# Performance work log

Hardware: AMD Instinct MI355X
Metric: run time of the kernel (lower is better)

Reference implementation:

```python
import jax, jax.numpy as jnp
import numpy as np

NUM_GROUPS = 32
EPS = 1e-5  # torch GroupNorm default


def group_norm(x, gamma, beta):
    # x: [B, C, T, H, W]; normalize each (b, t) frame per channel-group (CausalNormalize)
    B, C, T, H, W = x.shape
    xg = x.reshape(B, NUM_GROUPS, C // NUM_GROUPS, T, H, W)
    mu = xg.mean(axis=(2, 4, 5), keepdims=True)
    var = xg.var(axis=(2, 4, 5), keepdims=True)
    xn = ((xg - mu) * jax.lax.rsqrt(var + EPS)).reshape(B, C, T, H, W)
    return xn * gamma[None, :, None, None, None] + beta[None, :, None, None, None]


def setup_inputs() -> dict:
    key = jax.random.key(0)
    ks = jax.random.split(key, 8)
    B, C, T, H, W = 2, 512, 16, 32, 32
    S, D = 64, 1024  # context_T = 4 * T, context_dim
    wscale = 0.02
    return {
        "x": jax.random.normal(ks[0], (B, C, T, H, W), jnp.float32),
        "context": jax.random.normal(ks[1], (B, S, D), jnp.float32),
        "gamma": jnp.ones((C,), jnp.float32),
        "beta": jnp.zeros((C,), jnp.float32),
        "wq": jax.random.normal(ks[2], (C, C), jnp.float32) * wscale,
        "bq": jnp.zeros((C,), jnp.float32),
        "wkv": jax.random.normal(ks[3], (2 * C, D), jnp.float32) * wscale,
        "bkv": jnp.zeros((2 * C,), jnp.float32),
        "wo": jax.random.normal(ks[4], (C, C), jnp.float32) * wscale,
        "bo": jnp.zeros((C,), jnp.float32),
    }


def reference(x, context, gamma, beta, wq, bq, wkv, bkv, wo, bo):
    B, C, T, H, W = x.shape
    S = context.shape[1]
    n = S // T  # context frames per x frame (assert S % T == 0 in original)

    h = group_norm(x, gamma, beta)
    # q_proj: CausalConv3d with kernel 1, padding 0 == pointwise channel linear
    q = jnp.einsum('bcthw,oc->bothw', h, wq) + bq[None, :, None, None, None]

    kv = jnp.einsum('bsd,od->bso', context, wkv) + bkv  # [B, S, 2C]
    k, v = jnp.split(kv, 2, axis=-1)                    # each [B, S, C]

    # space2batch: [B,C,T,H,W] -> [B, H*W, T, C] (batch-major, queries per spatial pos)
    qb = q.transpose(0, 3, 4, 2, 1).reshape(B, H * W, T, C)

    # attention; kv broadcast over H*W done implicitly via einsum
    scores = jnp.einsum('bptc,bsc->bpts', qb, k) * (C ** -0.5)
    # block-causal mask: row i attends to context positions < (i+1)*n
    mask = jnp.arange(S)[None, :] < jnp.minimum((jnp.arange(T) + 1) * n, S)[:, None]
    scores = jnp.where(mask[None, None], scores, -jnp.inf)
    w = jax.nn.softmax(scores, axis=-1)
    o = jnp.einsum('bpts,bsc->bptc', w, v)              # [B, HW, T, C]

    # batch2space: back to [B, C, T, H, W]
    o = o.reshape(B, H, W, T, C).transpose(0, 4, 3, 1, 2)
    o = jnp.einsum('bcthw,oc->bothw', o, wo) + bo[None, :, None, None, None]
    return x + o
```

## Files before the change

### kernel.cpp

```cpp
#include <hip/hip_runtime.h>


typedef float    f32x4 __attribute__((ext_vector_type(4)));
typedef _Float16 half8 __attribute__((ext_vector_type(8)));
typedef _Float16 half4 __attribute__((ext_vector_type(4)));

#define GLB_AS __attribute__((address_space(1)))
#define LDS_AS __attribute__((address_space(3)))

__device__ __forceinline__ void gload_lds16(const void* g, void* l) {
  __builtin_amdgcn_global_load_lds((const GLB_AS void*)g, (LDS_AS void*)l, 16, 0, 0);
}

__global__ __launch_bounds__(256) void gn_stats(const float* __restrict__ x,
                                                float* __restrict__ muA,
                                                float* __restrict__ rsA)
{
  const int t = blockIdx.x, g = blockIdx.y, b = blockIdx.z;
  const int tid = threadIdx.x;
  float s1 = 0.f, s2 = 0.f;
#pragma unroll
  for (int c = 0; c < 16; ++c) {
    const long base = (((long)(b * 512 + g * 16 + c) * 16 + t) << 10) + tid * 4;
    const f32x4 v = *(const f32x4*)&x[base];
    s1 += v[0] + v[1] + v[2] + v[3];
    s2 += v[0] * v[0] + v[1] * v[1] + v[2] * v[2] + v[3] * v[3];
  }
  for (int o = 32; o; o >>= 1) { s1 += __shfl_down(s1, o); s2 += __shfl_down(s2, o); }
  __shared__ float r1[4], r2[4];
  const int w = tid >> 6;
  if ((tid & 63) == 0) { r1[w] = s1; r2[w] = s2; }
  __syncthreads();
  if (tid == 0) {
    const float a = r1[0] + r1[1] + r1[2] + r1[3];
    const float q = r2[0] + r2[1] + r2[2] + r2[3];
    const float mu = a * (1.f / 16384.f);
    const float var = q * (1.f / 16384.f) - mu * mu;
    const int idx = (b * 32 + g) * 16 + t;
    muA[idx] = mu;
    rsA[idx] = 1.f / sqrtf(var + 1e-5f);
  }
}

__global__ __launch_bounds__(256) void gn_apply(const float* __restrict__ x,
                                                const float* __restrict__ muA,
                                                const float* __restrict__ rsA,
                                                const float* __restrict__ gamma,
                                                const float* __restrict__ beta,
                                                _Float16* __restrict__ h)
{
  const int b = blockIdx.z;
  const int c0 = blockIdx.y * 64;
  const int p0 = blockIdx.x * 64;
  const int t = p0 >> 10;
  __shared__ float tile[64 * 65];
  const int tid = threadIdx.x;
  const int rr = tid >> 4;
  const int col4 = (tid & 15) * 4;
#pragma unroll
  for (int i = 0; i < 4; ++i) {
    const int r = i * 16 + rr;
    const int c = c0 + r;
    const int gi = (b * 32 + (c >> 4)) * 16 + t;
    const float s = rsA[gi] * gamma[c];
    const float o = beta[c] - muA[gi] * s;
    const f32x4 v = *(const f32x4*)&x[(((long)b * 512 + c) << 14) + p0 + col4];
    tile[r * 65 + col4 + 0] = v[0] * s + o;
    tile[r * 65 + col4 + 1] = v[1] * s + o;
    tile[r * 65 + col4 + 2] = v[2] * s + o;
    tile[r * 65 + col4 + 3] = v[3] * s + o;
  }
  __syncthreads();
  const int pr = tid >> 2;
  const int cs = (tid & 3) * 16;
  const long obase = (((long)b * 16384 + p0 + pr) << 9) + c0 + cs;
  half8 h0, h1;
#pragma unroll
  for (int j = 0; j < 16; ++j) {
    const _Float16 hi = (_Float16)tile[(cs + j) * 65 + pr];
    if (j < 8) h0[j] = hi; else h1[j - 8] = hi;
  }
  *(half8*)&h[obase]     = h0;
  *(half8*)&h[obase + 8] = h1;
}

__global__ void to_f16(const float* __restrict__ src, _Float16* __restrict__ dst, int n4)
{
  const int i = blockIdx.x * blockDim.x + threadIdx.x;
  if (i >= n4) return;
  const f32x4 v = *(const f32x4*)&src[i * 4];
  half4 hh;
#pragma unroll
  for (int j = 0; j < 4; ++j) hh[j] = (_Float16)v[j];
  *(half4*)&dst[i * 4] = hh;
}

__global__ __launch_bounds__(256) void kv_gemm(const float* __restrict__ ctx,
                                               const float* __restrict__ wkv,
                                               const float* __restrict__ bkv,
                                               _Float16* __restrict__ kOut,
                                               _Float16* __restrict__ vT)
{
  const int b = blockIdx.y;
  const int o0 = blockIdx.x * 16;
  const int tid = threadIdx.x, l = tid & 63, w = tid >> 6;
  __shared__ float cbuf[64 * 64];
  __shared__ float wbuf[16 * 64];
  float acc[4] = {0.f, 0.f, 0.f, 0.f};

  for (int dc = 0; dc < 16; ++dc) {
#pragma unroll
    for (int i = 0; i < 4; ++i) {
      const int lin = tid + i * 256;
      const int s = lin >> 4, c4 = lin & 15;
      *(f32x4*)&cbuf[s * 64 + ((c4 ^ (s & 15)) << 2)] =
          *(const f32x4*)&ctx[((long)(b * 64 + s) << 10) + dc * 64 + c4 * 4];
    }
    {
      const int o = tid >> 4, c4 = tid & 15;
      *(f32x4*)&wbuf[o * 64 + c4 * 4] =
          *(const f32x4*)&wkv[((long)(o0 + o) << 10) + dc * 64 + c4 * 4];
    }
    __syncthreads();
#pragma unroll
    for (int d4 = 0; d4 < 16; ++d4) {
      const f32x4 cv = *(const f32x4*)&cbuf[l * 64 + ((d4 ^ (l & 15)) << 2)];
#pragma unroll
      for (int j = 0; j < 4; ++j) {
        const f32x4 wv = *(const f32x4*)&wbuf[(w * 4 + j) * 64 + (d4 << 2)];
        acc[j] += cv[0] * wv[0] + cv[1] * wv[1] + cv[2] * wv[2] + cv[3] * wv[3];
      }
    }
    __syncthreads();
  }
#pragma unroll
  for (int j = 0; j < 4; ++j) {
    const int o = o0 + w * 4 + j;
    const float r = acc[j] + bkv[o];
    if (o < 512) kOut[((long)(b * 64 + l) << 9) + o] = (_Float16)r;
    else         vT[((long)(b * 512 + (o - 512)) << 6) + l] = (_Float16)r;
  }
}

#define BM 128
#define BN 128
#define BK 32

template <int BIAS_PER_N, int RESID, int OUT16>
__global__ __launch_bounds__(256) void gemm_f16(
    const _Float16* __restrict__ A, const _Float16* __restrict__ B,
    void* __restrict__ Cv, const float* __restrict__ bias, const float* __restrict__ resid,
    int K, int lda, int ldb, int ldc,
    long aBatch, long bBatch, long cBatch, long rBatch)
{
  __shared__ _Float16 sA[BM * BK];
  __shared__ _Float16 sB[BN * BK];
  const int tid = threadIdx.x;
  const int lane = tid & 63;
  const int w = tid >> 6;
  const int bz = blockIdx.z;
  const long m0 = (long)blockIdx.x * BM;
  const long n0 = (long)blockIdx.y * BN;
  const _Float16* pA = A + bz * aBatch + m0 * lda;
  const _Float16* pB = B + bz * bBatch + n0 * ldb;
  const int srow = lane >> 2;
  const int schunk = (lane & 3) * 8;
  const int wm = w >> 1, wn = w & 1;
  const int frow = lane & 15;
  const int fk = (lane >> 4) * 8;

  f32x4 acc[4][4] = {};

  for (int k0 = 0; k0 < K; k0 += BK) {
#pragma unroll
    for (int i = 0; i < 2; ++i) {
      const int r = w * 32 + i * 16 + srow;
      const int lbase = (w * 32 + i * 16) * BK;
      gload_lds16(pA + (long)r * lda + k0 + schunk, &sA[lbase]);
      gload_lds16(pB + (long)r * ldb + k0 + schunk, &sB[lbase]);
    }
    __syncthreads();
    half8 ah[4], bh[4];
#pragma unroll
    for (int mi = 0; mi < 4; ++mi)
      ah[mi] = *(const half8*)&sA[(wm * 64 + mi * 16 + frow) * BK + fk];
#pragma unroll
    for (int ni = 0; ni < 4; ++ni)
      bh[ni] = *(const half8*)&sB[(wn * 64 + ni * 16 + frow) * BK + fk];
#pragma unroll
    for (int mi = 0; mi < 4; ++mi)
#pragma unroll
      for (int ni = 0; ni < 4; ++ni)
        acc[mi][ni] = __builtin_amdgcn_mfma_f32_16x16x32_f16(ah[mi], bh[ni], acc[mi][ni], 0, 0, 0);
    __syncthreads();
  }

  const long cb = bz * cBatch;
  const long rb = bz * rBatch;
#pragma unroll
  for (int mi = 0; mi < 4; ++mi) {
#pragma unroll
    for (int ni = 0; ni < 4; ++ni) {
      const long row = m0 + wm * 64 + mi * 16 + (lane >> 4) * 4;
      const long col = n0 + wn * 64 + ni * 16 + (lane & 15);
#pragma unroll
      for (int j = 0; j < 4; ++j) {
        float v = acc[mi][ni][j];
        v += BIAS_PER_N ? bias[col] : bias[row + j];
        if (RESID) v += resid[rb + (row + j) * ldc + col];
        if (OUT16) ((_Float16*)Cv)[cb + (row + j) * ldc + col] = (_Float16)v;
        else       ((float*)Cv)[cb + (row + j) * ldc + col] = v;
      }
    }
  }
}

__global__ __launch_bounds__(256) void attn2(const _Float16* __restrict__ q,
                                             const _Float16* __restrict__ k,
                                             const _Float16* __restrict__ vT,
                                             _Float16* __restrict__ O)
{
  const int tid = threadIdx.x;
  const int l = tid & 63, w = tid >> 6;
  const int b = blockIdx.z, t = blockIdx.y;
  const int p0 = t * 1024 + blockIdx.x * 64 + w * 16;
  const int lim = (t + 1) * 4;
  const int nf = (t >> 2) + 1;
  const int ks = (t >> 3) + 1;
  const int cl = l & 15;
  const int g8 = (l >> 4) * 8;
  const int r4 = (l >> 4) * 4;

  __shared__ _Float16 wlds[4][16][72];

  f32x4 sc[4] = {};
  const _Float16* qb = q + (((long)(b * 16384 + p0 + cl)) << 9) + g8;
  const _Float16* kb = k + (((long)(b * 64 + cl)) << 9) + g8;
#pragma unroll
  for (int kk = 0; kk < 16; ++kk) {
    const half8 af = *(const half8*)(qb + kk * 32);
#pragma unroll
    for (int f = 0; f < 4; ++f)
      if (f < nf)
        sc[f] = __builtin_amdgcn_mfma_f32_16x16x32_f16(
            af, *(const half8*)(kb + f * (16 * 512) + kk * 32), sc[f], 0, 0, 0);
  }

  const float SCALE = 0.044194173824159216f;
  float ex[4][4], mj[4], sj[4];
#pragma unroll
  for (int j = 0; j < 4; ++j) {
    float mx = -1e30f;
#pragma unroll
    for (int f = 0; f < 4; ++f) {
      float v = sc[f][j] * SCALE;
      if (f * 16 + cl >= lim) v = -1e30f;
      ex[f][j] = v;
      mx = fmaxf(mx, v);
    }
    mj[j] = mx;
  }
#pragma unroll
  for (int o = 1; o < 16; o <<= 1)
#pragma unroll
    for (int j = 0; j < 4; ++j) mj[j] = fmaxf(mj[j], __shfl_xor(mj[j], o));
#pragma unroll
  for (int j = 0; j < 4; ++j) {
    float s = 0.f;
#pragma unroll
    for (int f = 0; f < 4; ++f) {
      const float e = __expf(ex[f][j] - mj[j]);
      ex[f][j] = e;
      s += e;
    }
    sj[j] = s;
  }
#pragma unroll
  for (int o = 1; o < 16; o <<= 1)
#pragma unroll
    for (int j = 0; j < 4; ++j) sj[j] += __shfl_xor(sj[j], o);
#pragma unroll
  for (int j = 0; j < 4; ++j) {
    const float inv = 1.f / sj[j];
#pragma unroll
    for (int f = 0; f < 4; ++f)
      wlds[w][r4 + j][f * 16 + cl] = (_Float16)(ex[f][j] * inv);
  }

  const half8 wa0 = *(const half8*)&wlds[w][cl][g8];
  const half8 wa1 = *(const half8*)&wlds[w][cl][32 + g8];
#pragma unroll
  for (int hf = 0; hf < 2; ++hf) {
    f32x4 oc[16] = {};
#pragma unroll
    for (int cf = 0; cf < 16; ++cf) {
      const _Float16* vb = vT + (((long)(b * 512 + hf * 256 + cf * 16 + cl)) << 6) + g8;
      oc[cf] = __builtin_amdgcn_mfma_f32_16x16x32_f16(wa0, *(const half8*)vb, oc[cf], 0, 0, 0);
      if (ks == 2)
        oc[cf] = __builtin_amdgcn_mfma_f32_16x16x32_f16(wa1, *(const half8*)(vb + 32), oc[cf], 0, 0, 0);
    }
#pragma unroll
    for (int cf = 0; cf < 16; ++cf)
#pragma unroll
      for (int j = 0; j < 4; ++j)
        O[(((long)(b * 16384 + p0 + r4 + j)) << 9) + hf * 256 + cf * 16 + cl] =
            (_Float16)oc[cf][j];
  }
}

extern "C" void kernel_launch(void* const* d_in, const int* in_sizes, int n_in,
                              void* d_out, int out_size, void* d_ws, size_t ws_size,
                              hipStream_t stream)
{
  (void)in_sizes; (void)n_in; (void)out_size; (void)ws_size;
  const float* x     = (const float*)d_in[0];
  const float* ctx   = (const float*)d_in[1];
  const float* gamma = (const float*)d_in[2];
  const float* beta  = (const float*)d_in[3];
  const float* wq    = (const float*)d_in[4];
  const float* bq    = (const float*)d_in[5];
  const float* wkv   = (const float*)d_in[6];
  const float* bkv   = (const float*)d_in[7];
  const float* wo    = (const float*)d_in[8];
  const float* bo    = (const float*)d_in[9];
  float* out = (float*)d_out;

  char* ws = (char*)d_ws;
  size_t off = 0;
  auto alloc = [&](size_t bytes) -> void* {
    void* p = ws + off;
    off += (bytes + 255) & ~(size_t)255;
    return p;
  };
  const long HPC = 8388608;
  _Float16* hF   = (_Float16*)alloc(2 * HPC * 2);
  _Float16* qF   = (_Float16*)alloc(2 * HPC * 2);
  _Float16* wqF  = (_Float16*)alloc(512 * 512 * 2);
  _Float16* woF  = (_Float16*)alloc(512 * 512 * 2);
  _Float16* kF   = (_Float16*)alloc(2 * 64 * 512 * 2);
  _Float16* vTF  = (_Float16*)alloc(2 * 512 * 64 * 2);
  float*    muA  = (float*)alloc(1024 * 4);
  float*    rsA  = (float*)alloc(1024 * 4);
  _Float16* oF   = hF;

  gn_stats<<<dim3(16, 32, 2), 256, 0, stream>>>(x, muA, rsA);
  gn_apply<<<dim3(256, 8, 2), 256, 0, stream>>>(x, muA, rsA, gamma, beta, hF);
  to_f16<<<dim3(256), 256, 0, stream>>>(wq, wqF, 65536);
  to_f16<<<dim3(256), 256, 0, stream>>>(wo, woF, 65536);
  kv_gemm<<<dim3(64, 2), 256, 0, stream>>>(ctx, wkv, bkv, kF, vTF);

  gemm_f16<1, 0, 1><<<dim3(128, 4, 2), 256, 0, stream>>>(
      hF, wqF, qF, bq, nullptr, 512, 512, 512, 512, HPC, 0, HPC, 0);

  attn2<<<dim3(16, 16, 2), 256, 0, stream>>>(qF, kF, vTF, oF);

  gemm_f16<0, 1, 0><<<dim3(4, 128, 2), 256, 0, stream>>>(
      woF, oF, out, bo, x, 512, 512, 512, 16384, 0, HPC, HPC, HPC);
}
```

Before: 301.0 us.

## Fuse GroupNorm stats/apply, double-buffer GEMM LDS, swizzle GEMM block order

```diff
diff --git a/kernel.cpp b/kernel.cpp
--- a/kernel.cpp
+++ b/kernel.cpp
@@ -12,76 +12,61 @@
   __builtin_amdgcn_global_load_lds((const GLB_AS void*)g, (LDS_AS void*)l, 16, 0, 0);
 }
 
-__global__ __launch_bounds__(256) void gn_stats(const float* __restrict__ x,
-                                                float* __restrict__ muA,
-                                                float* __restrict__ rsA)
-{
-  const int t = blockIdx.x, g = blockIdx.y, b = blockIdx.z;
-  const int tid = threadIdx.x;
-  float s1 = 0.f, s2 = 0.f;
-#pragma unroll
-  for (int c = 0; c < 16; ++c) {
-    const long base = (((long)(b * 512 + g * 16 + c) * 16 + t) << 10) + tid * 4;
-    const f32x4 v = *(const f32x4*)&x[base];
-    s1 += v[0] + v[1] + v[2] + v[3];
-    s2 += v[0] * v[0] + v[1] * v[1] + v[2] * v[2] + v[3] * v[3];
-  }
-  for (int o = 32; o; o >>= 1) { s1 += __shfl_down(s1, o); s2 += __shfl_down(s2, o); }
-  __shared__ float r1[4], r2[4];
-  const int w = tid >> 6;
-  if ((tid & 63) == 0) { r1[w] = s1; r2[w] = s2; }
-  __syncthreads();
-  if (tid == 0) {
-    const float a = r1[0] + r1[1] + r1[2] + r1[3];
-    const float q = r2[0] + r2[1] + r2[2] + r2[3];
-    const float mu = a * (1.f / 16384.f);
-    const float var = q * (1.f / 16384.f) - mu * mu;
-    const int idx = (b * 32 + g) * 16 + t;
-    muA[idx] = mu;
-    rsA[idx] = 1.f / sqrtf(var + 1e-5f);
-  }
-}
-
-__global__ __launch_bounds__(256) void gn_apply(const float* __restrict__ x,
-                                                const float* __restrict__ muA,
-                                                const float* __restrict__ rsA,
+__global__ __launch_bounds__(256) void gn_fused(const float* __restrict__ x,
                                                 const float* __restrict__ gamma,
                                                 const float* __restrict__ beta,
                                                 _Float16* __restrict__ h)
 {
-  const int b = blockIdx.z;
-  const int c0 = blockIdx.y * 64;
-  const int p0 = blockIdx.x * 64;
-  const int t = p0 >> 10;
-  __shared__ float tile[64 * 65];
+  const int t = blockIdx.x, g = blockIdx.y, b = blockIdx.z;
   const int tid = threadIdx.x;
-  const int rr = tid >> 4;
-  const int col4 = (tid & 15) * 4;
-#pragma unroll
-  for (int i = 0; i < 4; ++i) {
-    const int r = i * 16 + rr;
-    const int c = c0 + r;
-    const int gi = (b * 32 + (c >> 4)) * 16 + t;
-    const float s = rsA[gi] * gamma[c];
-    const float o = beta[c] - muA[gi] * s;
-    const f32x4 v = *(const f32x4*)&x[(((long)b * 512 + c) << 14) + p0 + col4];
-    tile[r * 65 + col4 + 0] = v[0] * s + o;
-    tile[r * 65 + col4 + 1] = v[1] * s + o;
-    tile[r * 65 + col4 + 2] = v[2] * s + o;
-    tile[r * 65 + col4 + 3] = v[3] * s + o;
-  }
+  __shared__ float tile[16 * 1028];
+  __shared__ float red[2][4];
+  const long xbase = ((long)((b * 512 + g * 16) * 16 + t)) << 10;
+
+  float s1 = 0.f, s2 = 0.f;
+#pragma unroll
+  for (int i = 0; i < 16; ++i) {
+    const int idx = i * 256 + tid;
+    const int c = idx >> 8;
+    const int p = (idx & 255) * 4;
+    const f32x4 v = *(const f32x4*)&x[xbase + ((long)c << 14) + p];
+    s1 += v[0] + v[1] + v[2] + v[3];
+    s2 += v[0] * v[0] + v[1] * v[1] + v[2] * v[2] + v[3] * v[3];
+    *(f32x4*)&tile[c * 1028 + p] = v;
+  }
+  for (int o = 32; o; o >>= 1) { s1 += __shfl_down(s1, o); s2 += __shfl_down(s2, o); }
+  if ((tid & 63) == 0) { red[0][tid >> 6] = s1; red[1][tid >> 6] = s2; }
   __syncthreads();
-  const int pr = tid >> 2;
-  const int cs = (tid & 3) * 16;
-  const long obase = (((long)b * 16384 + p0 + pr) << 9) + c0 + cs;
-  half8 h0, h1;
-#pragma unroll
-  for (int j = 0; j < 16; ++j) {
-    const _Float16 hi = (_Float16)tile[(cs + j) * 65 + pr];
-    if (j < 8) h0[j] = hi; else h1[j - 8] = hi;
-  }
-  *(half8*)&h[obase]     = h0;
-  *(half8*)&h[obase + 8] = h1;
+  const float a  = red[0][0] + red[0][1] + red[0][2] + red[0][3];
+  const float qq = red[1][0] + red[1][1] + red[1][2] + red[1][3];
+  const float mu = a * (1.f / 16384.f);
+  const float rs = rsqrtf(qq * (1.f / 16384.f) - mu * mu + 1e-5f);
+
+  float scv[16], ocv[16];
+#pragma unroll
+  for (int c4 = 0; c4 < 4; ++c4) {
+    const f32x4 gv = *(const f32x4*)&gamma[g * 16 + c4 * 4];
+    const f32x4 bv = *(const f32x4*)&beta[g * 16 + c4 * 4];
+#pragma unroll
+    for (int j = 0; j < 4; ++j) {
+      scv[c4 * 4 + j] = rs * gv[j];
+      ocv[c4 * 4 + j] = bv[j] - mu * scv[c4 * 4 + j];
+    }
+  }
+
+  const long hbase = (((long)b * 16384 + (long)t * 1024) << 9) + g * 16;
+#pragma unroll
+  for (int it = 0; it < 4; ++it) {
+    const int p = it * 256 + tid;
+    half8 h0, h1;
+#pragma unroll
+    for (int c = 0; c < 16; ++c) {
+      const _Float16 hv = (_Float16)(tile[c * 1028 + p] * scv[c] + ocv[c]);
+      if (c < 8) h0[c] = hv; else h1[c - 8] = hv;
+    }
+    *(half8*)&h[hbase + (long)p * 512]     = h0;
+    *(half8*)&h[hbase + (long)p * 512 + 8] = h1;
+  }
 }
 
 __global__ void to_f16(const float* __restrict__ src, _Float16* __restrict__ dst, int n4)
@@ -146,21 +131,35 @@
 #define BN 128
 #define BK 32
 
-template <int BIAS_PER_N, int RESID, int OUT16>
+template <int BIAS_PER_N, int RESID, int OUT16, int SWZ>
 __global__ __launch_bounds__(256) void gemm_f16(
     const _Float16* __restrict__ A, const _Float16* __restrict__ B,
     void* __restrict__ Cv, const float* __restrict__ bias, const float* __restrict__ resid,
     int K, int lda, int ldb, int ldc,
     long aBatch, long bBatch, long cBatch, long rBatch)
 {
-  __shared__ _Float16 sA[BM * BK];
-  __shared__ _Float16 sB[BN * BK];
+  __shared__ _Float16 sA[2][BM * BK];
+  __shared__ _Float16 sB[2][BN * BK];
   const int tid = threadIdx.x;
   const int lane = tid & 63;
   const int w = tid >> 6;
   const int bz = blockIdx.z;
-  const long m0 = (long)blockIdx.x * BM;
-  const long n0 = (long)blockIdx.y * BN;
+
+  int bx, by;
+  if (SWZ == 1) {
+    const int f = blockIdx.x;
+    const int nf = ((f & 7) << 6) | (f >> 3);
+    bx = nf & 3; by = nf >> 2;
+  } else if (SWZ == 2) {
+    const int f = blockIdx.x;
+    const int nf = ((f & 7) << 6) | (f >> 3);
+    bx = nf >> 2; by = nf & 3;
+  } else {
+    bx = blockIdx.x; by = blockIdx.y;
+  }
+
+  const long m0 = (long)bx * BM;
+  const long n0 = (long)by * BN;
   const _Float16* pA = A + bz * aBatch + m0 * lda;
   const _Float16* pB = B + bz * bBatch + n0 * ldb;
   const int srow = lane >> 2;
@@ -171,28 +170,35 @@
 
   f32x4 acc[4][4] = {};
 
-  for (int k0 = 0; k0 < K; k0 += BK) {
+  auto stage = [&](int buf, int k0) {
 #pragma unroll
     for (int i = 0; i < 2; ++i) {
       const int r = w * 32 + i * 16 + srow;
       const int lbase = (w * 32 + i * 16) * BK;
-      gload_lds16(pA + (long)r * lda + k0 + schunk, &sA[lbase]);
-      gload_lds16(pB + (long)r * ldb + k0 + schunk, &sB[lbase]);
-    }
-    __syncthreads();
+      gload_lds16(pA + (long)r * lda + k0 + schunk, &sA[buf][lbase]);
+      gload_lds16(pB + (long)r * ldb + k0 + schunk, &sB[buf][lbase]);
+    }
+  };
+
+  stage(0, 0);
+  __syncthreads();
+  int cur = 0;
+  for (int k0 = 0; k0 < K; k0 += BK) {
+    if (k0 + BK < K) stage(cur ^ 1, k0 + BK);
     half8 ah[4], bh[4];
 #pragma unroll
     for (int mi = 0; mi < 4; ++mi)
-      ah[mi] = *(const half8*)&sA[(wm * 64 + mi * 16 + frow) * BK + fk];
+      ah[mi] = *(const half8*)&sA[cur][(wm * 64 + mi * 16 + frow) * BK + fk];
 #pragma unroll
     for (int ni = 0; ni < 4; ++ni)
-      bh[ni] = *(const half8*)&sB[(wn * 64 + ni * 16 + frow) * BK + fk];
+      bh[ni] = *(const half8*)&sB[cur][(wn * 64 + ni * 16 + frow) * BK + fk];
 #pragma unroll
     for (int mi = 0; mi < 4; ++mi)
 #pragma unroll
       for (int ni = 0; ni < 4; ++ni)
         acc[mi][ni] = __builtin_amdgcn_mfma_f32_16x16x32_f16(ah[mi], bh[ni], acc[mi][ni], 0, 0, 0);
     __syncthreads();
+    cur ^= 1;
   }
 
   const long cb = bz * cBatch;
@@ -339,21 +345,18 @@
   _Float16* woF  = (_Float16*)alloc(512 * 512 * 2);
   _Float16* kF   = (_Float16*)alloc(2 * 64 * 512 * 2);
   _Float16* vTF  = (_Float16*)alloc(2 * 512 * 64 * 2);
-  float*    muA  = (float*)alloc(1024 * 4);
-  float*    rsA  = (float*)alloc(1024 * 4);
   _Float16* oF   = hF;
 
-  gn_stats<<<dim3(16, 32, 2), 256, 0, stream>>>(x, muA, rsA);
-  gn_apply<<<dim3(256, 8, 2), 256, 0, stream>>>(x, muA, rsA, gamma, beta, hF);
+  gn_fused<<<dim3(16, 32, 2), 256, 0, stream>>>(x, gamma, beta, hF);
   to_f16<<<dim3(256), 256, 0, stream>>>(wq, wqF, 65536);
   to_f16<<<dim3(256), 256, 0, stream>>>(wo, woF, 65536);
   kv_gemm<<<dim3(64, 2), 256, 0, stream>>>(ctx, wkv, bkv, kF, vTF);
 
-  gemm_f16<1, 0, 1><<<dim3(128, 4, 2), 256, 0, stream>>>(
+  gemm_f16<1, 0, 1, 2><<<dim3(512, 1, 2), 256, 0, stream>>>(
       hF, wqF, qF, bq, nullptr, 512, 512, 512, 512, HPC, 0, HPC, 0);
 
   attn2<<<dim3(16, 16, 2), 256, 0, stream>>>(qF, kF, vTF, oF);
 
-  gemm_f16<0, 1, 0><<<dim3(4, 128, 2), 256, 0, stream>>>(
+  gemm_f16<0, 1, 0, 1><<<dim3(512, 1, 2), 256, 0, stream>>>(
       woF, oF, out, bo, x, 512, 512, 512, 16384, 0, HPC, HPC, HPC);
 }
```

Result: faster. 291.4 us (-3.2%).
